# Kernel tuning notes

Hardware: AMD Instinct MI355X
Metric: run time of the kernel (lower is better)

Reference implementation:

```python
import jax, jax.numpy as jnp
import numpy as np

V, B, P, NE = 8, 128, 512, 75
NU = 0.1
EPS = 1e-5
SQRT2 = float(np.sqrt(2.0))


def transform(p):
    # UpperDiagonalThresholdedLogTransform: rotate 45deg, log-threshold the persistence axis
    s = (p[..., 0] + p[..., 1]) / SQRT2
    y = (p[..., 1] - p[..., 0]) / SQRT2
    y = jnp.where(y <= NU, jnp.log(jnp.maximum(y, 1e-12) / NU) + NU, y)
    return jnp.stack([s, y], -1)


def setup_inputs() -> dict:
    key = jax.random.key(0)
    ks = jax.random.split(key, 16)
    u = jax.random.uniform(ks[0], (V, B, P, 2), dtype=jnp.float32)
    birth = u[..., 0] * 0.5
    death = birth + u[..., 1] * 0.5 + 0.01  # death > birth
    points = jnp.stack([birth, death], -1)
    lengths = jax.random.randint(ks[1], (V, B), 64, P + 1)
    cu = jax.random.uniform(ks[2], (V, NE, 2), dtype=jnp.float32)
    cb = cu[..., 0] * 0.5
    cd = cb + cu[..., 1] * 0.5 + 0.01
    centers = transform(jnp.stack([cb, cd], -1))  # transformed center init, per direction
    sharpness = jnp.ones((V, NE, 2), jnp.float32) * 4.0
    r = lambda k, s, sc: jax.random.normal(k, s, jnp.float32) * sc
    return dict(
        points=points, lengths=lengths, centers=centers, sharpness=sharpness,
        conv1_w=r(ks[3], (V, 16, 3), 0.3), conv2_w=r(ks[4], (V, 4, 16), 0.3),
        l1_w=r(ks[5], (V, 25, NE), 0.1), l1_b=r(ks[6], (V, 25), 0.01),
        bn1_g=jnp.ones((V, 25), jnp.float32), bn1_b=jnp.zeros((V, 25), jnp.float32),
        l2_w=r(ks[7], (V, 25, 25), 0.2), l2_b=r(ks[8], (V, 25), 0.01),
        fc1_w=r(ks[9], (100, V * 25), 0.07), fc1_b=r(ks[10], (100,), 0.01),
        fc1_bn_g=jnp.ones((100,), jnp.float32), fc1_bn_b=jnp.zeros((100,), jnp.float32),
        fc2_w=r(ks[11], (70, 100), 0.1), fc2_b=r(ks[12], (70,), 0.01))


def reference(points, lengths, centers, sharpness, conv1_w, conv2_w, l1_w, l1_b,
              bn1_g, bn1_b, l2_w, l2_b, fc1_w, fc1_b, fc1_bn_g, fc1_bn_b, fc2_w, fc2_b):
    tp = transform(points)                                   # [V,B,P,2]
    mask = (jnp.arange(P)[None, None, :] < lengths[:, :, None]).astype(tp.dtype)  # [V,B,P]
    outs = []
    for i in range(V):  # fixed small loop over PHT directions
        idx = jnp.array([(i - 1) % V, i, (i + 1) % V])       # neighbor directions (cyclic)
        pts3 = tp[idx]                                       # [3,B,P,2]
        m3 = mask[idx]                                       # [3,B,P]
        # soft structure element: exp(-sum_d sharpness_d * (p_d - c_d)^2), masked sum over points
        diff = pts3[:, :, :, None, :] - centers[i][None, None, None]   # [3,B,P,NE,2]
        resp = jnp.exp(-jnp.sum(sharpness[i] * diff * diff, -1)) * m3[..., None]
        sl = jnp.transpose(jnp.sum(resp, 2), (1, 0, 2))      # [B,3,NE]
        h = jnp.einsum('fc,bcn->bfn', conv1_w[i], sl)        # conv1d k=1: 3->16
        h = jnp.einsum('gf,bfn->bgn', conv2_w[i], h)         # conv1d k=1: 16->4
        h = jnp.max(h, 1)                                    # [B,NE]
        a = h @ l1_w[i].T + l1_b[i]                          # [B,25]
        a = (a - a.mean(0)) / jnp.sqrt(a.var(0) + EPS) * bn1_g[i] + bn1_b[i]
        a = jax.nn.relu(a @ l2_w[i].T + l2_b[i])             # dropout = identity (eval)
        outs.append(a)
    x = jnp.concatenate(outs, 1)                             # [B, V*25]
    x = x @ fc1_w.T + fc1_b
    x = (x - x.mean(0)) / jnp.sqrt(x.var(0) + EPS) * fc1_bn_g + fc1_bn_b
    return x @ fc2_w.T + fc2_b                               # [B,70]
```

## Files before the change

### kernel.cpp

```cpp
#include <hip/hip_runtime.h>
#include <math.h>

#define V 8
#define B 128
#define P 512
#define NE 75

static constexpr float NU = 0.1f;
static constexpr float EPS = 1e-5f;
static constexpr float INV_SQRT2 = 0.70710678118654752440f;
static constexpr float L2E = 1.4426950408889634f;

typedef float v4f __attribute__((ext_vector_type(4)));

__device__ __forceinline__ float fast_exp2(float x) {
#if __has_builtin(__builtin_amdgcn_exp2f)
  return __builtin_amdgcn_exp2f(x);
#else
  return exp2f(x);
#endif
}

__device__ __forceinline__ v4f v4fma(v4f a, v4f b, v4f c) {
#if __has_builtin(__builtin_elementwise_fma)
  return __builtin_elementwise_fma(a, b, c);
#else
  v4f r;
  r.x = fmaf(a.x, b.x, c.x); r.y = fmaf(a.y, b.y, c.y);
  r.z = fmaf(a.z, b.z, c.z); r.w = fmaf(a.w, b.w, c.w);
  return r;
#endif
}

__global__ __launch_bounds__(256, 4) void k_structure(
    const float2* __restrict__ pts2,
    const int* __restrict__ lengths,
    const float* __restrict__ centers,
    const float* __restrict__ sharp,
    const float* __restrict__ c1w,
    const float* __restrict__ c2w,
    const float* __restrict__ l1w,
    const float* __restrict__ l1b,
    float* __restrict__ A1t) {
  int i = blockIdx.x >> 7;
  int b = blockIdx.x & 127;
  int t = threadIdx.x;

  __shared__ float sS[3][P], sY[3][P];
  __shared__ float slb[3][NE];
  __shared__ float hn[NE];

  int d0 = (i + V - 1) & (V - 1), d1 = i, d2 = (i + 1) & (V - 1);
  int len0 = lengths[d0 * B + b];
  int len1 = lengths[d1 * B + b];
  int len2 = lengths[d2 * B + b];

  for (int u = t; u < 3 * P; u += 256) {
    int jj = u >> 9;
    int pp = u & (P - 1);
    int d   = (jj == 0) ? d0 : (jj == 1) ? d1 : d2;
    int len = (jj == 0) ? len0 : (jj == 1) ? len1 : len2;
    float2 q = pts2[((size_t)d * B + b) * P + pp];
    float s = (q.x + q.y) * INV_SQRT2;
    float y = (q.y - q.x) * INV_SQRT2;
    if (y <= NU) y = __logf(fmaxf(y, 1e-12f) * 10.0f) + NU;
    if (pp >= len) { s = 1e9f; y = 1e9f; }
    sS[jj][pp] = s;
    sY[jj][pp] = y;
  }

  int w = t >> 6, l = t & 63;
  int j, n;
  bool active;
  if (w < 3) {
    j = w;
    n = l;
    active = true;
  } else {
    active = (l < 33);
    int jl = l / 11;
    if (!active) jl = 2;
    j = jl;
    n = active ? (64 + (l - jl * 11)) : 74;
  }

  int ci = (i * NE + n) * 2;
  float a  = sharp[ci],   c  = sharp[ci + 1];
  float cs = centers[ci], cy = centers[ci + 1];
  float nA = -a * L2E;
  float nC = -c * L2E;
  float Bsc = 2.0f * a * cs * L2E;
  float Byc = 2.0f * c * cy * L2E;
  float nD = -(a * cs * cs + c * cy * cy) * L2E;
  v4f nA4 = {nA, nA, nA, nA}, nC4 = {nC, nC, nC, nC};
  v4f Bs4 = {Bsc, Bsc, Bsc, Bsc}, By4 = {Byc, Byc, Byc, Byc};
  v4f nD4 = {nD, nD, nD, nD};

  int mx = (w == 0) ? len0
         : (w == 1) ? len1
         : (w == 2) ? len2 : max(len0, max(len1, len2));
  int trip = (mx + 7) & ~7;

  __syncthreads();

  float ac0 = 0.f, ac1 = 0.f, ac2 = 0.f, ac3 = 0.f;
  float ac4 = 0.f, ac5 = 0.f, ac6 = 0.f, ac7 = 0.f;
  for (int p = 0; p < trip; p += 8) {
    v4f Sa = *(const v4f*)&sS[j][p], Sb = *(const v4f*)&sS[j][p + 4];
    v4f Ya = *(const v4f*)&sY[j][p], Yb = *(const v4f*)&sY[j][p + 4];
    v4f ua = v4fma(nA4, Sa, Bs4), ub = v4fma(nA4, Sb, Bs4);
    v4f va = v4fma(nC4, Ya, By4), vb = v4fma(nC4, Yb, By4);
    v4f ta = v4fma(Sa, ua, nD4),  tb = v4fma(Sb, ub, nD4);
    v4f argA = v4fma(Ya, va, ta), argB = v4fma(Yb, vb, tb);
    ac0 += fast_exp2(argA.x);
    ac1 += fast_exp2(argA.y);
    ac2 += fast_exp2(argA.z);
    ac3 += fast_exp2(argA.w);
    ac4 += fast_exp2(argB.x);
    ac5 += fast_exp2(argB.y);
    ac6 += fast_exp2(argB.z);
    ac7 += fast_exp2(argB.w);
  }
  float accv = ((ac0 + ac1) + (ac2 + ac3)) + ((ac4 + ac5) + (ac6 + ac7));

  if (active) slb[j][n] = accv;
  __syncthreads();

  if (t < NE) {
    float s0 = slb[0][t], s1 = slb[1][t], s2 = slb[2][t];
    float a0 = 0, a1 = 0, a2 = 0, a3 = 0;
#pragma unroll
    for (int f = 0; f < 16; ++f) {
      float w0 = c1w[(i * 16 + f) * 3 + 0];
      float w1 = c1w[(i * 16 + f) * 3 + 1];
      float w2 = c1w[(i * 16 + f) * 3 + 2];
      float h1 = fmaf(w0, s0, fmaf(w1, s1, w2 * s2));
      a0 = fmaf(c2w[(i * 4 + 0) * 16 + f], h1, a0);
      a1 = fmaf(c2w[(i * 4 + 1) * 16 + f], h1, a1);
      a2 = fmaf(c2w[(i * 4 + 2) * 16 + f], h1, a2);
      a3 = fmaf(c2w[(i * 4 + 3) * 16 + f], h1, a3);
    }
    hn[t] = fmaxf(fmaxf(a0, a1), fmaxf(a2, a3));
  }
  __syncthreads();

  if (t < 25) {
    float acc = l1b[i * 25 + t];
    const float* wgt = l1w + ((size_t)i * 25 + t) * NE;
#pragma unroll 5
    for (int m = 0; m < NE; ++m) acc = fmaf(wgt[m], hn[m], acc);
    A1t[((size_t)(i * 25 + t)) * B + b] = acc;
  }
}

__global__ __launch_bounds__(256) void k_tail1(
    const float* __restrict__ A1t, const float* __restrict__ g1,
    const float* __restrict__ b1, const float* __restrict__ l2w,
    const float* __restrict__ l2b, const float* __restrict__ fc1w,
    const float* __restrict__ fc1b, float* __restrict__ Yt) {
  int b = blockIdx.x;
  int t = threadIdx.x;
  __shared__ float xin[200];
  __shared__ float Xl[200];

  if (t < 200) {
    const float4* col = (const float4*)(A1t + (size_t)t * B);
    float4 s4 = {0, 0, 0, 0}, q4 = {0, 0, 0, 0};
#pragma unroll
    for (int u = 0; u < B / 4; ++u) {
      float4 v = col[u];
      s4.x += v.x; s4.y += v.y; s4.z += v.z; s4.w += v.w;
      q4.x = fmaf(v.x, v.x, q4.x); q4.y = fmaf(v.y, v.y, q4.y);
      q4.z = fmaf(v.z, v.z, q4.z); q4.w = fmaf(v.w, v.w, q4.w);
    }
    float s = (s4.x + s4.y) + (s4.z + s4.w);
    float q = (q4.x + q4.y) + (q4.z + q4.w);
    float m = s * (1.0f / B);
    float var = q * (1.0f / B) - m * m;
    float r = rsqrtf(var + EPS);
    float v = A1t[(size_t)t * B + b];
    xin[t] = (v - m) * r * g1[t] + b1[t];
  }
  __syncthreads();
  if (t < 200) {
    int i = t / 25;
    float acc = l2b[t];
    const float* w = l2w + (size_t)t * 25;
    const float* x = xin + i * 25;
#pragma unroll
    for (int jj = 0; jj < 25; ++jj) acc = fmaf(w[jj], x[jj], acc);
    Xl[t] = fmaxf(acc, 0.0f);
  }
  __syncthreads();
  if (t < 100) {
    float acc = fc1b[t];
    const float* w = fc1w + (size_t)t * 200;
#pragma unroll 8
    for (int q = 0; q < 200; ++q) acc = fmaf(w[q], Xl[q], acc);
    Yt[(size_t)t * B + b] = acc;
  }
}

__global__ __launch_bounds__(128) void k_tail2(
    const float* __restrict__ Yt, const float* __restrict__ g2,
    const float* __restrict__ b2, const float* __restrict__ fc2w,
    const float* __restrict__ fc2b, float* __restrict__ out) {
  int b = blockIdx.x;
  int t = threadIdx.x;
  __shared__ float yin[100];
  if (t < 100) {
    const float4* col = (const float4*)(Yt + (size_t)t * B);
    float4 s4 = {0, 0, 0, 0}, q4 = {0, 0, 0, 0};
#pragma unroll
    for (int u = 0; u < B / 4; ++u) {
      float4 v = col[u];
      s4.x += v.x; s4.y += v.y; s4.z += v.z; s4.w += v.w;
      q4.x = fmaf(v.x, v.x, q4.x); q4.y = fmaf(v.y, v.y, q4.y);
      q4.z = fmaf(v.z, v.z, q4.z); q4.w = fmaf(v.w, v.w, q4.w);
    }
    float s = (s4.x + s4.y) + (s4.z + s4.w);
    float q = (q4.x + q4.y) + (q4.z + q4.w);
    float m = s * (1.0f / B);
    float var = q * (1.0f / B) - m * m;
    float r = rsqrtf(var + EPS);
    float v = Yt[(size_t)t * B + b];
    yin[t] = (v - m) * r * g2[t] + b2[t];
  }
  __syncthreads();
  if (t < 70) {
    float acc = fc2b[t];
    const float* w = fc2w + (size_t)t * 100;
#pragma unroll 4
    for (int m = 0; m < 100; ++m) acc = fmaf(w[m], yin[m], acc);
    out[(size_t)b * 70 + t] = acc;
  }
}

extern "C" void kernel_launch(void* const* d_in, const int* in_sizes, int n_in,
                              void* d_out, int out_size, void* d_ws, size_t ws_size,
                              hipStream_t stream) {
  const float2* pts2   = (const float2*)d_in[0];
  const int*   lengths = (const int*)d_in[1];
  const float* centers = (const float*)d_in[2];
  const float* sharp   = (const float*)d_in[3];
  const float* c1w     = (const float*)d_in[4];
  const float* c2w     = (const float*)d_in[5];
  const float* l1w     = (const float*)d_in[6];
  const float* l1b     = (const float*)d_in[7];
  const float* bn1g    = (const float*)d_in[8];
  const float* bn1b    = (const float*)d_in[9];
  const float* l2w     = (const float*)d_in[10];
  const float* l2b     = (const float*)d_in[11];
  const float* fc1w    = (const float*)d_in[12];
  const float* fc1b    = (const float*)d_in[13];
  const float* fbn_g   = (const float*)d_in[14];
  const float* fbn_b   = (const float*)d_in[15];
  const float* fc2w    = (const float*)d_in[16];
  const float* fc2b    = (const float*)d_in[17];
  float* out = (float*)d_out;

  float* A1t = (float*)d_ws;
  float* Yt  = A1t + 200 * B;

  k_structure<<<dim3(V * B), dim3(256), 0, stream>>>(
      pts2, lengths, centers, sharp, c1w, c2w, l1w, l1b, A1t);
  k_tail1<<<dim3(B), dim3(256), 0, stream>>>(
      A1t, bn1g, bn1b, l2w, l2b, fc1w, fc1b, Yt);
  k_tail2<<<dim3(B), dim3(128), 0, stream>>>(
      Yt, fbn_g, fbn_b, fc2w, fc2b, out);
}
```

Measured before the change: 44.16 us.

## Fuse tail kernels via last-block atomic counter to drop a launch

Merges the two tail kernels into one by having every block increment a global atomic counter after writing its Yt slice; the block that arrives last computes the second batch-norm and the fc2 layer for the whole batch. This removes one kernel launch and its inter-kernel gap. In exchange, the final fc2 work for all 128 batch rows runs serially on a single block, using 51 KB of shared memory for the normalized activations. The counter is never reset and relies on modulo-128 wraparound across calls, assuming zeroed workspace.

```diff
diff --git a/kernel.cpp b/kernel.cpp
--- a/kernel.cpp
+++ b/kernel.cpp
@@ -153,15 +153,20 @@
   }
 }
 
-__global__ __launch_bounds__(256) void k_tail1(
+__global__ __launch_bounds__(256) void k_tail12(
     const float* __restrict__ A1t, const float* __restrict__ g1,
     const float* __restrict__ b1, const float* __restrict__ l2w,
     const float* __restrict__ l2b, const float* __restrict__ fc1w,
-    const float* __restrict__ fc1b, float* __restrict__ Yt) {
+    const float* __restrict__ fc1b, const float* __restrict__ g2,
+    const float* __restrict__ b2, const float* __restrict__ fc2w,
+    const float* __restrict__ fc2b, float* __restrict__ Yt,
+    unsigned int* __restrict__ cnt, float* __restrict__ out) {
   int b = blockIdx.x;
   int t = threadIdx.x;
   __shared__ float xin[200];
   __shared__ float Xl[200];
+  __shared__ float yn[100][128];
+  __shared__ int isLast;
 
   if (t < 200) {
     const float4* col = (const float4*)(A1t + (size_t)t * B);
@@ -199,40 +204,45 @@
     for (int q = 0; q < 200; ++q) acc = fmaf(w[q], Xl[q], acc);
     Yt[(size_t)t * B + b] = acc;
   }
-}
-
-__global__ __launch_bounds__(128) void k_tail2(
-    const float* __restrict__ Yt, const float* __restrict__ g2,
-    const float* __restrict__ b2, const float* __restrict__ fc2w,
-    const float* __restrict__ fc2b, float* __restrict__ out) {
-  int b = blockIdx.x;
-  int t = threadIdx.x;
-  __shared__ float yin[100];
+
+  __threadfence();
+  __syncthreads();
+  if (t == 0) {
+    unsigned int old = atomicAdd(cnt, 1u);
+    isLast = ((old & 127u) == 127u) ? 1 : 0;
+  }
+  __syncthreads();
+  if (!isLast) return;
+
+  __threadfence();
   if (t < 100) {
-    const float4* col = (const float4*)(Yt + (size_t)t * B);
-    float4 s4 = {0, 0, 0, 0}, q4 = {0, 0, 0, 0};
-#pragma unroll
-    for (int u = 0; u < B / 4; ++u) {
-      float4 v = col[u];
-      s4.x += v.x; s4.y += v.y; s4.z += v.z; s4.w += v.w;
-      q4.x = fmaf(v.x, v.x, q4.x); q4.y = fmaf(v.y, v.y, q4.y);
-      q4.z = fmaf(v.z, v.z, q4.z); q4.w = fmaf(v.w, v.w, q4.w);
-    }
-    float s = (s4.x + s4.y) + (s4.z + s4.w);
-    float q = (q4.x + q4.y) + (q4.z + q4.w);
+    const float* row = Yt + (size_t)t * B;
+    float s = 0.f, q = 0.f;
+#pragma unroll 8
+    for (int u = 0; u < B; ++u) {
+      float v = row[u];
+      s += v;
+      q = fmaf(v, v, q);
+    }
     float m = s * (1.0f / B);
     float var = q * (1.0f / B) - m * m;
     float r = rsqrtf(var + EPS);
-    float v = Yt[(size_t)t * B + b];
-    yin[t] = (v - m) * r * g2[t] + b2[t];
-  }
-  __syncthreads();
-  if (t < 70) {
-    float acc = fc2b[t];
-    const float* w = fc2w + (size_t)t * 100;
+    float gg = g2[t], bb = b2[t];
+    for (int u = 0; u < B; ++u)
+      yn[t][u] = (row[u] - m) * r * gg + bb;
+  }
+  __syncthreads();
+  {
+    int bb = t & 127;
+    int o0 = (t >> 7) * 35;
+    for (int oo = 0; oo < 35; ++oo) {
+      int o = o0 + oo;
+      float acc = fc2b[o];
+      const float* w = fc2w + (size_t)o * 100;
 #pragma unroll 4
-    for (int m = 0; m < 100; ++m) acc = fmaf(w[m], yin[m], acc);
-    out[(size_t)b * 70 + t] = acc;
+      for (int f = 0; f < 100; ++f) acc = fmaf(w[f], yn[f][bb], acc);
+      out[(size_t)bb * 70 + o] = acc;
+    }
   }
 }
 
@@ -261,11 +271,11 @@
 
   float* A1t = (float*)d_ws;
   float* Yt  = A1t + 200 * B;
+  unsigned int* cnt = (unsigned int*)(Yt + 100 * B);
 
   k_structure<<<dim3(V * B), dim3(256), 0, stream>>>(
       pts2, lengths, centers, sharp, c1w, c2w, l1w, l1b, A1t);
-  k_tail1<<<dim3(B), dim3(256), 0, stream>>>(
-      A1t, bn1g, bn1b, l2w, l2b, fc1w, fc1b, Yt);
-  k_tail2<<<dim3(B), dim3(128), 0, stream>>>(
-      Yt, fbn_g, fbn_b, fc2w, fc2b, out);
-}
+  k_tail12<<<dim3(B), dim3(256), 0, stream>>>(
+      A1t, bn1g, bn1b, l2w, l2b, fc1w, fc1b, fbn_g, fbn_b, fc2w, fc2b,
+      Yt, cnt, out);
+}
```

Result: slower. 121.7 us (+175.6%).

## Split point reduction across two thread halves with 512-thread blocks

Applied to the files above, without the earlier changes.

Structure kernel now uses 512 threads per block. Each (direction, center) pair is handled by two threads that process alternating 8-point chunks, and their partial sums are combined through shared memory. This replaces the old layout in which a fourth wave handled the leftover centers while iterating to the max length. It also swaps the exp and log builtins for inline v_exp_f32 and v_log_f32 asm. The aim is to cut the serial exp loop length per thread and balance work across waves, at the cost of an extra barrier and reduction step.

```diff
diff --git a/kernel.cpp b/kernel.cpp
--- a/kernel.cpp
+++ b/kernel.cpp
@@ -10,15 +10,19 @@
 static constexpr float EPS = 1e-5f;
 static constexpr float INV_SQRT2 = 0.70710678118654752440f;
 static constexpr float L2E = 1.4426950408889634f;
+static constexpr float LN2 = 0.69314718055994530942f;
 
 typedef float v4f __attribute__((ext_vector_type(4)));
 
 __device__ __forceinline__ float fast_exp2(float x) {
-#if __has_builtin(__builtin_amdgcn_exp2f)
-  return __builtin_amdgcn_exp2f(x);
-#else
-  return exp2f(x);
-#endif
+  float r;
+  asm("v_exp_f32 %0, %1" : "=v"(r) : "v"(x));
+  return r;
+}
+__device__ __forceinline__ float fast_log2(float x) {
+  float r;
+  asm("v_log_f32 %0, %1" : "=v"(r) : "v"(x));
+  return r;
 }
 
 __device__ __forceinline__ v4f v4fma(v4f a, v4f b, v4f c) {
@@ -32,7 +36,7 @@
 #endif
 }
 
-__global__ __launch_bounds__(256, 4) void k_structure(
+__global__ __launch_bounds__(512, 2) void k_structure(
     const float2* __restrict__ pts2,
     const int* __restrict__ lengths,
     const float* __restrict__ centers,
@@ -47,6 +51,7 @@
   int t = threadIdx.x;
 
   __shared__ float sS[3][P], sY[3][P];
+  __shared__ float part[450];
   __shared__ float slb[3][NE];
   __shared__ float hn[NE];
 
@@ -55,7 +60,7 @@
   int len1 = lengths[d1 * B + b];
   int len2 = lengths[d2 * B + b];
 
-  for (int u = t; u < 3 * P; u += 256) {
+  for (int u = t; u < 3 * P; u += 512) {
     int jj = u >> 9;
     int pp = u & (P - 1);
     int d   = (jj == 0) ? d0 : (jj == 1) ? d1 : d2;
@@ -63,26 +68,18 @@
     float2 q = pts2[((size_t)d * B + b) * P + pp];
     float s = (q.x + q.y) * INV_SQRT2;
     float y = (q.y - q.x) * INV_SQRT2;
-    if (y <= NU) y = __logf(fmaxf(y, 1e-12f) * 10.0f) + NU;
+    if (y <= NU) y = fast_log2(fmaxf(y, 1e-12f) * 10.0f) * LN2 + NU;
     if (pp >= len) { s = 1e9f; y = 1e9f; }
     sS[jj][pp] = s;
     sY[jj][pp] = y;
   }
 
-  int w = t >> 6, l = t & 63;
-  int j, n;
-  bool active;
-  if (w < 3) {
-    j = w;
-    n = l;
-    active = true;
-  } else {
-    active = (l < 33);
-    int jl = l / 11;
-    if (!active) jl = 2;
-    j = jl;
-    n = active ? (64 + (l - jl * 11)) : 74;
-  }
+  bool active = (t < 450);
+  int q = active ? t : 449;
+  int half = (q >= 225) ? 1 : 0;
+  int jn = q - half * 225;
+  int j = jn / 75;
+  int n = jn - j * 75;
 
   int ci = (i * NE + n) * 2;
   float a  = sharp[ci],   c  = sharp[ci + 1];
@@ -96,16 +93,18 @@
   v4f Bs4 = {Bsc, Bsc, Bsc, Bsc}, By4 = {Byc, Byc, Byc, Byc};
   v4f nD4 = {nD, nD, nD, nD};
 
-  int mx = (w == 0) ? len0
-         : (w == 1) ? len1
-         : (w == 2) ? len2 : max(len0, max(len1, len2));
-  int trip = (mx + 7) & ~7;
+  int mylen = (j == 0) ? len0 : (j == 1) ? len1 : len2;
+  int lmax = mylen;
+#pragma unroll
+  for (int o = 32; o; o >>= 1) lmax = max(lmax, __shfl_xor(lmax, o));
+  int nc8 = (lmax + 7) >> 3;
 
   __syncthreads();
 
   float ac0 = 0.f, ac1 = 0.f, ac2 = 0.f, ac3 = 0.f;
   float ac4 = 0.f, ac5 = 0.f, ac6 = 0.f, ac7 = 0.f;
-  for (int p = 0; p < trip; p += 8) {
+  for (int cch = 0; cch < nc8; cch += 2) {
+    int p = (cch + half) * 8;
     v4f Sa = *(const v4f*)&sS[j][p], Sb = *(const v4f*)&sS[j][p + 4];
     v4f Ya = *(const v4f*)&sY[j][p], Yb = *(const v4f*)&sY[j][p + 4];
     v4f ua = v4fma(nA4, Sa, Bs4), ub = v4fma(nA4, Sb, Bs4);
@@ -123,7 +122,13 @@
   }
   float accv = ((ac0 + ac1) + (ac2 + ac3)) + ((ac4 + ac5) + (ac6 + ac7));
 
-  if (active) slb[j][n] = accv;
+  if (active) part[t] = accv;
+  __syncthreads();
+
+  if (t < 225) {
+    int jj = t / 75, nn = t - jj * 75;
+    slb[jj][nn] = part[t] + part[t + 225];
+  }
   __syncthreads();
 
   if (t < NE) {
@@ -262,7 +267,7 @@
   float* A1t = (float*)d_ws;
   float* Yt  = A1t + 200 * B;
 
-  k_structure<<<dim3(V * B), dim3(256), 0, stream>>>(
+  k_structure<<<dim3(V * B), dim3(512), 0, stream>>>(
       pts2, lengths, centers, sharp, c1w, c2w, l1w, l1b, A1t);
   k_tail1<<<dim3(B), dim3(256), 0, stream>>>(
       A1t, bn1g, bn1b, l2w, l2b, fc1w, fc1b, Yt);
```

After: 45.21 us. 2.4% more time.
